# Kernel tuning notes

Hardware: AMD Instinct MI355X
Metric: run time of the kernel (lower is better)

The kernel has to match this reference:

```python
import jax, jax.numpy as jnp
import numpy as np

B, T, N, F = 4, 24, 1024, 96
H, HD = 3, 32      # spatial GATConv: 3 heads, head-dim 32 (averaged -> 32 per branch, 3 branches -> 96)
GH, GHD = 4, 24    # GroupedGAT: 4 heads concatenated -> 96
E = 8192           # edges per graph


def setup_inputs() -> dict:
    key = jax.random.key(0)
    ks = jax.random.split(key, 24)
    s_in = 1.0 / np.sqrt(F)
    def gat_params(k):
        k1, k2, k3, k4 = jax.random.split(k, 4)
        return (jax.random.normal(k1, (F, H * HD), jnp.float32) * s_in,
                jax.random.normal(k2, (H, HD), jnp.float32) * 0.1,
                jax.random.normal(k3, (H, HD), jnp.float32) * 0.1,
                jax.random.normal(k4, (H, HD), jnp.float32) * 0.02)
    W_d, al_d, ar_d, b_d = gat_params(ks[3])
    W_m, al_m, ar_m, b_m = gat_params(ks[4])
    W_s, al_s, ar_s, b_s = gat_params(ks[5])
    inp = {
        "input": jax.random.normal(ks[0], (B, T, N, F), jnp.float32),
        "spatial_embedding": jax.random.normal(ks[1], (B, T, N, F), jnp.float32),
        "temporal_embedding": jax.random.normal(ks[2], (B, T, N, F), jnp.float32),
        "src_d": jax.random.randint(ks[6], (E,), 0, N, jnp.int32),
        "dst_d": (jnp.arange(E) % N).astype(jnp.int32),
        "src_m": jax.random.randint(ks[7], (E,), 0, N, jnp.int32),
        "dst_m": (jnp.arange(E) % N).astype(jnp.int32),
        "src_s": jax.random.randint(ks[8], (E,), 0, N, jnp.int32),
        "dst_s": (jnp.arange(E) % N).astype(jnp.int32),
        "W_d": W_d, "al_d": al_d, "ar_d": ar_d, "b_d": b_d,
        "W_m": W_m, "al_m": al_m, "ar_m": ar_m, "b_m": b_m,
        "W_s": W_s, "al_s": al_s, "ar_s": ar_s, "b_s": b_s,
        "Wg": jax.random.normal(ks[9], (F, GH * GHD), jnp.float32) * s_in,
        "agl": jax.random.normal(ks[10], (GH, GHD), jnp.float32) * 0.1,
        "agr": jax.random.normal(ks[11], (GH, GHD), jnp.float32) * 0.1,
        "Wf": jax.random.normal(ks[12], (2 * F, F), jnp.float32) * (1.0 / np.sqrt(2 * F)),
        "bf": jnp.zeros((F,), jnp.float32),
    }
    return inp


def _gat(x, src, dst, W, al, ar, b):
    # x: (N, K, F) node features with K = T*B batched feature slots
    K = x.shape[1]
    h = (x @ W).reshape(N, K, H, HD)                       # (N,K,H,HD)
    el = (h * al).sum(-1)                                  # (N,K,H)
    er = (h * ar).sum(-1)
    e = jax.nn.leaky_relu(el[src] + er[dst], 0.2)          # (E,K,H)
    emax = jax.ops.segment_max(e, dst, num_segments=N)
    emax = jnp.where(jnp.isfinite(emax), emax, 0.0)
    ex = jnp.exp(e - emax[dst])
    denom = jax.ops.segment_sum(ex, dst, num_segments=N)
    alpha = ex / (denom[dst] + 1e-9)                       # edge softmax over incoming edges
    out = jax.ops.segment_sum(h[src] * alpha[..., None], dst, num_segments=N)
    return (out + b).mean(2)                               # average heads -> (N,K,HD)


def reference(input, spatial_embedding, temporal_embedding,
              src_d, dst_d, src_m, dst_m, src_s, dst_s,
              W_d, al_d, ar_d, b_d, W_m, al_m, ar_m, b_m, W_s, al_s, ar_s, b_s,
              Wg, agl, agr, Wf, bf):
    # ---------------- SpatialBlock ----------------
    residual_s = input                                     # input_dim == output_dim
    x_in = input + spatial_embedding
    # torch: input.transpose(0,2).reshape(N,-1,F) -> slot order is (t,b)
    x = jnp.transpose(x_in, (2, 1, 0, 3)).reshape(N, T * B, F)
    xd = _gat(x, src_d, dst_d, W_d, al_d, ar_d, b_d)
    xm = _gat(x, src_m, dst_m, W_m, al_m, ar_m, b_m)
    xs = _gat(x, src_s, dst_s, W_s, al_s, ar_s, b_s)
    x_attn = jnp.concatenate([xd, xm, xs], axis=-1)        # (N, T*B, 3*HD=F)
    # torch: transpose(0,1).reshape(batch,T,N,-1)  (keeps original (t,b) slot order quirk)
    x_attn = jnp.transpose(x_attn, (1, 0, 2)).reshape(B, T, N, F)
    cov0 = spatial_embedding[:, 0]                         # (B,N,F)
    attn_S = jax.nn.softmax(cov0 @ jnp.swapaxes(cov0, 1, 2), axis=2)  # (B,N,N)
    # NOTE: embedding_x branch in SpatialBlock is dead code (out is overwritten); skipped.
    spatial = residual_s + x_attn

    # ---------------- TemporalBlock ----------------
    residual_t = input
    xt = jnp.swapaxes(input, 1, 2).reshape(B * N, T, F)    # (B*N, T, F), index k=b*N+n
    # GroupedGAT: dense multi-head GAT over the T=period_num time steps
    hg = (xt @ Wg).reshape(B * N, T, GH, GHD)
    elg = (hg * agl).sum(-1)                               # (BN,T,GH)
    erg = (hg * agr).sum(-1)
    eg = jax.nn.leaky_relu(elg[:, :, None, :] + erg[:, None, :, :], 0.2)  # (BN,Ti,Tj,GH)
    alphag = jax.nn.softmax(eg, axis=2)
    xg = jnp.einsum('kijh,kjhd->kihd', alphag, hg).reshape(B * N, T, GH * GHD)
    covT = temporal_embedding[:, :, 0]                     # (B,T,F)
    attn_T = jax.nn.softmax(covT @ jnp.swapaxes(covT, 1, 2), axis=1)      # softmax over dim=1 as in torch
    # torch: attn.repeat(N,1,1) paired with x of batch index b*N+n -> uses attn[(b*N+n) % B]
    idx = (jnp.arange(B * N) % B)
    emb = jnp.einsum('kij,kjf->kif', attn_T[idx], xt)      # (BN,T,F)
    xg = xg * jax.nn.sigmoid(emb)
    xg = jnp.swapaxes(xg.reshape(B, N, T, F), 1, 2)        # (B,T,N,F)
    temporal = residual_t + xg

    # ---------------- Fusion ----------------
    z = jax.nn.sigmoid(jnp.concatenate([spatial, temporal], axis=-1) @ Wf + bf)
    out = z * spatial + (1.0 - z) * temporal + input
    return out, attn_S
```

## Files before the change

kernel.cpp:

```cpp
#include <hip/hip_runtime.h>
#include <hip/hip_bf16.h>

typedef long long i64;
typedef __attribute__((ext_vector_type(8))) short short8b;
typedef __attribute__((ext_vector_type(4))) short short4b;
typedef __attribute__((ext_vector_type(4))) float f32x4;

union U8 { short8b v; ushort s[8]; };
union U4 { short4b v; ushort s[4]; };

static __device__ __forceinline__ float bs2f(ushort u) {
    union { unsigned int i; float f; } x; x.i = ((unsigned int)u) << 16; return x.f;
}
static __device__ __forceinline__ ushort f2bs(float f) {
    __hip_bfloat16 h = __float2bfloat16(f);
    return *reinterpret_cast<ushort*>(&h);
}
static __device__ __forceinline__ void mfma_bf16(f32x4& acc, short8b a, short8b b) {
    asm volatile("v_mfma_f32_16x16x32_bf16 %0, %1, %2, %0" : "+v"(acc) : "v"(a), "v"(b));
}
static __device__ __forceinline__ void mfma_fence() {
    asm volatile("s_nop 7\n\ts_nop 7\n\ts_nop 7");
}


__global__ __launch_bounds__(256) void prep_weights_kernel(
        const float* __restrict__ Wd, const float* __restrict__ Wm,
        const float* __restrict__ Ws, const float* __restrict__ Wg,
        const float* __restrict__ Wf,
        const float* __restrict__ ald, const float* __restrict__ ard,
        const float* __restrict__ alm, const float* __restrict__ arm,
        const float* __restrict__ als, const float* __restrict__ ars,
        const float* __restrict__ agl, const float* __restrict__ agr,
        ushort* __restrict__ wtab) {
    int idx = blockIdx.x * 256 + threadIdx.x;
    if (idx >= 61440) return;
    if (idx < 43008) {
        int w = idx / 10752, rem = idx - w * 10752;
        int c = rem / 96, k = rem - c * 96;
        float v;
        if (w < 3) {
            const float* W = (w == 0) ? Wd : (w == 1) ? Wm : Ws;
            if (c < 96) {
                v = W[k * 96 + c];
            } else {
                int j = c - 96, h = j >> 1;
                const float* a = (j & 1) ? ((w == 0) ? ard : (w == 1) ? arm : ars)
                                         : ((w == 0) ? ald : (w == 1) ? alm : als);
                v = 0.f;
                for (int d = 0; d < 32; ++d) v += W[k * 96 + h * 32 + d] * a[h * 32 + d];
            }
        } else {
            if (c < 96) {
                v = Wg[k * 96 + c];
            } else {
                int j = c - 96, g = j & 3;
                const float* a = (j >> 2) ? agr : agl;
                v = 0.f;
                for (int d = 0; d < 24; ++d) v += Wg[k * 96 + g * 24 + d] * a[g * 24 + d];
            }
        }
        wtab[w * 10752 + c * 96 + k] = f2bs(v);
    } else {
        int rem = idx - 43008;
        int c = rem / 192, k = rem - c * 192;
        wtab[43008 + c * 192 + k] = f2bs(Wf[k * 96 + c]);
    }
}

__global__ __launch_bounds__(256) void build_x_kernel(const float* __restrict__ inp,
                                                      const float* __restrict__ spat,
                                                      ushort* __restrict__ x) {
    int i4 = blockIdx.x * 256 + threadIdx.x;
    int q = i4 % 24;
    int r = i4 / 24;
    int n = r & 1023, bt = r >> 10;
    int t = bt % 24, b = bt / 24;
    int k = t * 4 + b;
    float4 a = ((const float4*)inp)[i4];
    float4 s = ((const float4*)spat)[i4];
    U4 u;
    u.s[0] = f2bs(a.x + s.x); u.s[1] = f2bs(a.y + s.y);
    u.s[2] = f2bs(a.z + s.z); u.s[3] = f2bs(a.w + s.w);
    *(short4b*)&x[((i64)((k << 10) | n)) * 96 + q * 4] = u.v;
}

__global__ __launch_bounds__(256) void gemm96_mfma_kernel(const ushort* __restrict__ X,
                                                          const ushort* __restrict__ wt,
                                                          ushort* __restrict__ Ho,
                                                          float* __restrict__ el,
                                                          float* __restrict__ er) {
    __shared__ ushort Xs[128 * 104];
    __shared__ ushort Wt[112 * 104];
    int tid = threadIdx.x;
    i64 row0 = (i64)blockIdx.x * 128;
    for (int i = tid; i < 1344; i += 256) {
        int c = i / 12, kg = i - c * 12;
        *(short8b*)&Wt[c * 104 + kg * 8] = *(const short8b*)&wt[c * 96 + kg * 8];
    }
    for (int i = tid; i < 1536; i += 256) {
        int r = i / 12, q = i - r * 12;
        *(short8b*)&Xs[r * 104 + q * 8] = *(const short8b*)&X[(row0 + r) * 96 + q * 8];
    }
    __syncthreads();
    int wid = tid >> 6, lane = tid & 63;
    int lr = lane & 15, lk = lane >> 4;
    f32x4 acc[2][7];
#pragma unroll
    for (int m = 0; m < 2; ++m)
#pragma unroll
        for (int c = 0; c < 7; ++c) acc[m][c] = (f32x4){0.f, 0.f, 0.f, 0.f};
    const ushort* xa = &Xs[(wid * 32 + lr) * 104 + lk * 8];
    const ushort* wb = &Wt[lr * 104 + lk * 8];
#pragma unroll
    for (int ks = 0; ks < 3; ++ks) {
        short8b a0 = *(const short8b*)(xa + ks * 32);
        short8b a1 = *(const short8b*)(xa + 16 * 104 + ks * 32);
#pragma unroll
        for (int c = 0; c < 7; ++c) {
            short8b b = *(const short8b*)(wb + c * 16 * 104 + ks * 32);
            mfma_bf16(acc[0][c], a0, b);
            mfma_bf16(acc[1][c], a1, b);
        }
    }
    mfma_fence();
#pragma unroll
    for (int m = 0; m < 2; ++m) {
#pragma unroll
        for (int c = 0; c < 6; ++c)
#pragma unroll
            for (int r = 0; r < 4; ++r) {
                i64 row = row0 + wid * 32 + m * 16 + lk * 4 + r;
                Ho[row * 96 + c * 16 + lr] = f2bs(acc[m][c][r]);
            }
        if (lr < 6) {
            float* dst = (lr & 1) ? er : el;
            int h = lr >> 1;
#pragma unroll
            for (int r = 0; r < 4; ++r) {
                i64 row = row0 + wid * 32 + m * 16 + lk * 4 + r;
                dst[row * 3 + h] = acc[m][6][r];
            }
        }
    }
}

__global__ __launch_bounds__(256) void gemm96_hg_mfma_kernel(const float* __restrict__ inp,
                                                             const ushort* __restrict__ wt,
                                                             ushort* __restrict__ Ho,
                                                             float* __restrict__ elg,
                                                             float* __restrict__ erg) {
    __shared__ ushort Xs[128 * 104];
    __shared__ ushort Wt[112 * 104];
    int tid = threadIdx.x;
    i64 row0 = (i64)blockIdx.x * 128;
    for (int i = tid; i < 1344; i += 256) {
        int c = i / 12, kg = i - c * 12;
        *(short8b*)&Wt[c * 104 + kg * 8] = *(const short8b*)&wt[c * 96 + kg * 8];
    }
    for (int i = tid; i < 3072; i += 256) {
        int r = i / 24, q = i - r * 24;
        int row = (int)row0 + r;
        int kk = row / 24, t = row - kk * 24;
        int b = kk >> 10, n = kk & 1023;
        float4 v = ((const float4*)inp)[((i64)(((b * 24 + t) << 10) | n)) * 24 + q];
        U4 u;
        u.s[0] = f2bs(v.x); u.s[1] = f2bs(v.y); u.s[2] = f2bs(v.z); u.s[3] = f2bs(v.w);
        *(short4b*)&Xs[r * 104 + q * 4] = u.v;
    }
    __syncthreads();
    int wid = tid >> 6, lane = tid & 63;
    int lr = lane & 15, lk = lane >> 4;
    f32x4 acc[2][7];
#pragma unroll
    for (int m = 0; m < 2; ++m)
#pragma unroll
        for (int c = 0; c < 7; ++c) acc[m][c] = (f32x4){0.f, 0.f, 0.f, 0.f};
    const ushort* xa = &Xs[(wid * 32 + lr) * 104 + lk * 8];
    const ushort* wb = &Wt[lr * 104 + lk * 8];
#pragma unroll
    for (int ks = 0; ks < 3; ++ks) {
        short8b a0 = *(const short8b*)(xa + ks * 32);
        short8b a1 = *(const short8b*)(xa + 16 * 104 + ks * 32);
#pragma unroll
        for (int c = 0; c < 7; ++c) {
            short8b b = *(const short8b*)(wb + c * 16 * 104 + ks * 32);
            mfma_bf16(acc[0][c], a0, b);
            mfma_bf16(acc[1][c], a1, b);
        }
    }
    mfma_fence();
#pragma unroll
    for (int m = 0; m < 2; ++m) {
#pragma unroll
        for (int c = 0; c < 6; ++c)
#pragma unroll
            for (int r = 0; r < 4; ++r) {
                i64 row = row0 + wid * 32 + m * 16 + lk * 4 + r;
                Ho[row * 96 + c * 16 + lr] = f2bs(acc[m][c][r]);
            }
        if (lr < 8) {
            float* dst = (lr >> 2) ? erg : elg;
            int g = lr & 3;
#pragma unroll
            for (int r = 0; r < 4; ++r) {
                i64 row = row0 + wid * 32 + m * 16 + lk * 4 + r;
                dst[row * 4 + g] = acc[m][6][r];
            }
        }
    }
}

__global__ __launch_bounds__(256) void gat_agg_kernel(const ushort* __restrict__ H2,
                                                      const float* __restrict__ el,
                                                      const float* __restrict__ er,
                                                      const int* __restrict__ src,
                                                      const float* __restrict__ bv,
                                                      ushort* __restrict__ xattn,
                                                      int g) {
    int tid = threadIdx.x;
    int pp = tid >> 3, l8 = tid & 7;
    int p = blockIdx.x * 32 + pp;
    int k = p >> 10, n = p & 1023;
    int d0 = l8 * 4;
    i64 kb = (i64)(k << 10);
    int s_own = src[n + l8 * 1024];
    const float* elp = &el[(kb | s_own) * 3];
    const float* erp = &er[(kb | n) * 3];
    float e[3], m[3];
#pragma unroll
    for (int h = 0; h < 3; ++h) {
        float ev = elp[h] + erp[h];
        e[h] = ev >= 0.f ? ev : 0.2f * ev;
        m[h] = e[h];
    }
#pragma unroll
    for (int mask = 1; mask < 8; mask <<= 1) {
#pragma unroll
        for (int h = 0; h < 3; ++h) m[h] = fmaxf(m[h], __shfl_xor(m[h], mask, 8));
    }
    float pex[3], S[3];
#pragma unroll
    for (int h = 0; h < 3; ++h) { pex[h] = expf(e[h] - m[h]); S[h] = pex[h]; }
#pragma unroll
    for (int mask = 1; mask < 8; mask <<= 1) {
#pragma unroll
        for (int h = 0; h < 3; ++h) S[h] += __shfl_xor(S[h], mask, 8);
    }
    float w[3];
#pragma unroll
    for (int h = 0; h < 3; ++h) w[h] = pex[h] / (S[h] + 1e-9f);
    float acc[4] = {0.f, 0.f, 0.f, 0.f};
#pragma unroll
    for (int j = 0; j < 8; ++j) {
        int sj = __shfl(s_own, j, 8);
        float a0 = __shfl(w[0], j, 8);
        float a1 = __shfl(w[1], j, 8);
        float a2 = __shfl(w[2], j, 8);
        const ushort* hp = &H2[(kb | sj) * 96 + d0];
        U4 h0, h1, h2;
        h0.v = *(const short4b*)&hp[0];
        h1.v = *(const short4b*)&hp[32];
        h2.v = *(const short4b*)&hp[64];
#pragma unroll
        for (int c = 0; c < 4; ++c)
            acc[c] += a0 * bs2f(h0.s[c]) + a1 * bs2f(h1.s[c]) + a2 * bs2f(h2.s[c]);
    }
    float4 b0 = *(const float4*)&bv[d0];
    float4 b1 = *(const float4*)&bv[32 + d0];
    float4 b2 = *(const float4*)&bv[64 + d0];
    float bsum[4] = {b0.x + b1.x + b2.x, b0.y + b1.y + b2.y,
                     b0.z + b1.z + b2.z, b0.w + b1.w + b2.w};
    U4 u;
#pragma unroll
    for (int c = 0; c < 4; ++c) u.s[c] = f2bs((acc[c] + bsum[c]) * (1.f / 3.f));
    *(short4b*)&xattn[(kb | n) * 96 + g * 32 + d0] = u.v;
}

__global__ __launch_bounds__(256) void attn_scores_kernel(const float* __restrict__ spat,
                                                          float* __restrict__ attnS) {
    int bid = blockIdx.x;
    int b = bid >> 8;
    int i0 = ((bid >> 4) & 15) * 64;
    int j0 = (bid & 15) * 64;
    const float* C = spat + (i64)b * 24 * 1024 * 96;
    __shared__ __align__(16) float As[64 * 100];
    __shared__ __align__(16) float Bs[64 * 100];
    int tid = threadIdx.x;
    float4* As4 = (float4*)As;
    float4* Bs4 = (float4*)Bs;
    const float4* Ai = (const float4*)(C + (i64)i0 * 96);
    const float4* Bj = (const float4*)(C + (i64)j0 * 96);
    for (int i = tid; i < 1536; i += 256) {
        int row = i / 24, q = i - row * 24;
        As4[row * 25 + q] = Ai[i];
        Bs4[row * 25 + q] = Bj[i];
    }
    __syncthreads();
    int tj = tid & 15, ti = tid >> 4;
    float acc[4][4];
#pragma unroll
    for (int r = 0; r < 4; ++r)
#pragma unroll
        for (int s = 0; s < 4; ++s) acc[r][s] = 0.f;
    for (int k4 = 0; k4 < 24; ++k4) {
        float4 a[4], bv[4];
#pragma unroll
        for (int r = 0; r < 4; ++r) a[r] = As4[(ti * 4 + r) * 25 + k4];
#pragma unroll
        for (int s = 0; s < 4; ++s) bv[s] = Bs4[(s * 16 + tj) * 25 + k4];
#pragma unroll
        for (int r = 0; r < 4; ++r)
#pragma unroll
            for (int s = 0; s < 4; ++s)
                acc[r][s] += a[r].x * bv[s].x + a[r].y * bv[s].y + a[r].z * bv[s].z + a[r].w * bv[s].w;
    }
#pragma unroll
    for (int r = 0; r < 4; ++r) {
        i64 orow = ((i64)(b << 10) + i0 + ti * 4 + r) * 1024 + j0;
#pragma unroll
        for (int s = 0; s < 4; ++s) attnS[orow + s * 16 + tj] = acc[r][s];
    }
}

__global__ __launch_bounds__(256) void attn_softmax_kernel(float* __restrict__ attnS) {
    i64 base = (i64)blockIdx.x * 1024;
    float4* row4 = (float4*)(attnS + base);
    int tid = threadIdx.x;
    float4 v = row4[tid];
    __shared__ float red[256];
    float m = fmaxf(fmaxf(v.x, v.y), fmaxf(v.z, v.w));
    red[tid] = m;
    __syncthreads();
    for (int st = 128; st > 0; st >>= 1) {
        if (tid < st) red[tid] = fmaxf(red[tid], red[tid + st]);
        __syncthreads();
    }
    m = red[0];
    __syncthreads();
    v.x = expf(v.x - m); v.y = expf(v.y - m); v.z = expf(v.z - m); v.w = expf(v.w - m);
    red[tid] = v.x + v.y + v.z + v.w;
    __syncthreads();
    for (int st = 128; st > 0; st >>= 1) {
        if (tid < st) red[tid] += red[tid + st];
        __syncthreads();
    }
    float inv = 1.f / red[0];
    v.x *= inv; v.y *= inv; v.z *= inv; v.w *= inv;
    row4[tid] = v;
}

__global__ __launch_bounds__(576) void attn_t_kernel(const float* __restrict__ temp,
                                                     float* __restrict__ attnT) {
    int b = blockIdx.x;
    int tid = threadIdx.x;
    __shared__ float cs[24][96];
    __shared__ float M[24][24];
    for (int i = tid; i < 2304; i += 576) {
        int r = i / 96, f = i - r * 96;
        cs[r][f] = temp[((i64)(b * 24 + r)) * 1024 * 96 + f];
    }
    __syncthreads();
    int i = tid / 24, j = tid - i * 24;
    float s = 0.f;
#pragma unroll
    for (int f = 0; f < 96; ++f) s += cs[i][f] * cs[j][f];
    M[i][j] = s;
    __syncthreads();
    float m = -1e30f;
#pragma unroll
    for (int i2 = 0; i2 < 24; ++i2) m = fmaxf(m, M[i2][j]);
    float sum = 0.f;
#pragma unroll
    for (int i2 = 0; i2 < 24; ++i2) sum += expf(M[i2][j] - m);
    attnT[((i64)b * 24 + i) * 24 + j] = expf(M[i][j] - m) / sum;
}

__global__ __launch_bounds__(576) void sig_kernel(const float* __restrict__ inp,
                                                  const float* __restrict__ attnT,
                                                  ushort* __restrict__ sig) {
    int kk = blockIdx.x;
    int b = kk >> 10, n = kk & 1023;
    __shared__ __align__(16) float xs[24 * 100];
    __shared__ float ats[576];
    int tid = threadIdx.x;
    {
        int r = tid / 24, q = tid - (tid / 24) * 24;
        *(float4*)&xs[r * 100 + q * 4] =
            ((const float4*)inp)[(((i64)(b * 24 + r)) << 10 | n) * 24 + q];
        ats[tid] = attnT[(kk & 3) * 576 + tid];
    }
    __syncthreads();
    int i = tid / 24, f4 = tid - (tid / 24) * 24;
    const float* ap = &ats[i * 24];
    float4 acc = {0.f, 0.f, 0.f, 0.f};
#pragma unroll
    for (int j = 0; j < 24; ++j) {
        float a = ap[j];
        float4 v = *(const float4*)&xs[j * 100 + f4 * 4];
        acc.x += a * v.x; acc.y += a * v.y; acc.z += a * v.z; acc.w += a * v.w;
    }
    U4 o;
    o.s[0] = f2bs(1.f / (1.f + expf(-acc.x)));
    o.s[1] = f2bs(1.f / (1.f + expf(-acc.y)));
    o.s[2] = f2bs(1.f / (1.f + expf(-acc.z)));
    o.s[3] = f2bs(1.f / (1.f + expf(-acc.w)));
    *(short4b*)&sig[(i64)kk * 2304 + i * 96 + f4 * 4] = o.v;
}

__global__ __launch_bounds__(192) void xg_kernel(const ushort* __restrict__ hg,
                                                 const float* __restrict__ elgb,
                                                 const float* __restrict__ ergb,
                                                 const ushort* __restrict__ sig,
                                                 ushort* __restrict__ gated) {
    int kk = blockIdx.x;
    __shared__ __align__(16) ushort hgs[24 * 96];
    __shared__ __align__(16) float alphaT[4 * 24 * 32];
    __shared__ __align__(16) float elg[24][4], erg[24][4];
    int tid = threadIdx.x;
    for (int i = tid; i < 576; i += 192)
        *(short4b*)&hgs[i * 4] = *(const short4b*)&hg[(i64)kk * 2304 + i * 4];
    for (int i = tid; i < 48; i += 192) {
        int r = i >> 1;
        if (i & 1) *(float4*)&erg[r][0] = ((const float4*)ergb)[(i64)kk * 24 + r];
        else       *(float4*)&elg[r][0] = ((const float4*)elgb)[(i64)kk * 24 + r];
    }
    __syncthreads();
    {
        int i = tid >> 3, g = (tid >> 1) & 3, half = tid & 1;
        int j0 = half * 12;
        float eli = elg[i][g];
        float ev[12];
        float m = -1e30f;
#pragma unroll
        for (int j = 0; j < 12; ++j) {
            float e = eli + erg[j0 + j][g];
            e = e >= 0.f ? e : 0.2f * e;
            ev[j] = e;
            m = fmaxf(m, e);
        }
        m = fmaxf(m, __shfl_xor(m, 1));
        float sum = 0.f;
#pragma unroll
        for (int j = 0; j < 12; ++j) { ev[j] = expf(ev[j] - m); sum += ev[j]; }
        sum += __shfl_xor(sum, 1);
        float inv = 1.f / sum;
        int slot = ((i / 3) * 4 + (i - (i / 3) * 3)) ^ (g << 3);
#pragma unroll
        for (int j = 0; j < 12; ++j) alphaT[g * 768 + (j0 + j) * 32 + slot] = ev[j] * inv;
    }
    __syncthreads();
    int ig = tid / 24, f4 = tid - (tid / 24) * 24;
    int g = f4 / 6;
    float4 xg0 = {0,0,0,0}, xg1 = {0,0,0,0}, xg2 = {0,0,0,0};
    const float* aT = &alphaT[g * 768 + ((ig * 4) ^ (g << 3))];
#pragma unroll
    for (int j = 0; j < 24; ++j) {
        U4 uh; uh.v = *(const short4b*)&hgs[j * 96 + f4 * 4];
        float4 a4 = *(const float4*)&aT[j * 32];
        float h0 = bs2f(uh.s[0]), h1 = bs2f(uh.s[1]), h2 = bs2f(uh.s[2]), h3 = bs2f(uh.s[3]);
        xg0.x += a4.x * h0; xg0.y += a4.x * h1; xg0.z += a4.x * h2; xg0.w += a4.x * h3;
        xg1.x += a4.y * h0; xg1.y += a4.y * h1; xg1.z += a4.y * h2; xg1.w += a4.y * h3;
        xg2.x += a4.z * h0; xg2.y += a4.z * h1; xg2.z += a4.z * h2; xg2.w += a4.z * h3;
    }
    i64 obase = (i64)kk * 2304 + f4 * 4;
#pragma unroll
    for (int r = 0; r < 3; ++r) {
        float4 xg = (r == 0) ? xg0 : (r == 1) ? xg1 : xg2;
        i64 off = obase + (i64)(ig * 3 + r) * 96;
        U4 us; us.v = *(const short4b*)&sig[off];
        U4 o;
        o.s[0] = f2bs(xg.x * bs2f(us.s[0]));
        o.s[1] = f2bs(xg.y * bs2f(us.s[1]));
        o.s[2] = f2bs(xg.z * bs2f(us.s[2]));
        o.s[3] = f2bs(xg.w * bs2f(us.s[3]));
        *(short4b*)&gated[off] = o.v;
    }
}

__global__ __launch_bounds__(384) void fusion_mfma_kernel(const float* __restrict__ inp,
                                                          const ushort* __restrict__ xattn,
                                                          const ushort* __restrict__ gated,
                                                          const ushort* __restrict__ wtf,
                                                          const float* __restrict__ bfv,
                                                          float* __restrict__ outb) {
    extern __shared__ __align__(16) ushort dynlds[];
    ushort* Xs = dynlds;
    ushort* Wt = dynlds + 96 * 200;
    float* zbuf = (float*)Wt;
    int tid = threadIdx.x;
    i64 row0 = (i64)blockIdx.x * 96;
    for (int i = tid; i < 2304; i += 384) {
        int c = i / 24, kg = i - c * 24;
        *(short8b*)&Wt[c * 200 + kg * 8] = *(const short8b*)&wtf[c * 192 + kg * 8];
    }
    for (int i = tid; i < 1152; i += 384) {
        int r = i / 12, q = i - r * 12;
        i64 grow = row0 + r;
        int n = (int)(grow & 1023);
        int bt = (int)(grow >> 10);
        int t = bt % 24, b = bt / 24;
        float4 iv0 = ((const float4*)inp)[grow * 24 + q * 2];
        float4 iv1 = ((const float4*)inp)[grow * 24 + q * 2 + 1];
        U8 xa; xa.v = *(const short8b*)&xattn[grow * 96 + q * 8];
        U8 gd; gd.v = *(const short8b*)&gated[(((i64)((b << 10) | n)) * 24 + t) * 96 + q * 8];
        float ivf[8] = {iv0.x, iv0.y, iv0.z, iv0.w, iv1.x, iv1.y, iv1.z, iv1.w};
        U8 sp, tm;
#pragma unroll
        for (int j = 0; j < 8; ++j) {
            sp.s[j] = f2bs(ivf[j] + bs2f(xa.s[j]));
            tm.s[j] = f2bs(ivf[j] + bs2f(gd.s[j]));
        }
        *(short8b*)&Xs[r * 200 + q * 8] = sp.v;
        *(short8b*)&Xs[r * 200 + 96 + q * 8] = tm.v;
    }
    __syncthreads();
    int wid = tid >> 6, lane = tid & 63;
    int lr = lane & 15, lk = lane >> 4;
    f32x4 acc[6];
#pragma unroll
    for (int c = 0; c < 6; ++c) acc[c] = (f32x4){0.f, 0.f, 0.f, 0.f};
    const ushort* xa = &Xs[(wid * 16 + lr) * 200 + lk * 8];
    const ushort* wb = &Wt[lr * 200 + lk * 8];
#pragma unroll
    for (int ks = 0; ks < 6; ++ks) {
        short8b a = *(const short8b*)(xa + ks * 32);
#pragma unroll
        for (int c = 0; c < 6; ++c) {
            short8b b = *(const short8b*)(wb + c * 16 * 200 + ks * 32);
            mfma_bf16(acc[c], a, b);
        }
    }
    mfma_fence();
    __syncthreads();
#pragma unroll
    for (int c = 0; c < 6; ++c) {
        int col = c * 16 + lr;
        float bfc = bfv[col];
#pragma unroll
        for (int r = 0; r < 4; ++r) {
            int lrow = wid * 16 + lk * 4 + r;
            zbuf[lrow * 100 + col] = 1.f / (1.f + expf(-(acc[c][r] + bfc)));
        }
    }
    __syncthreads();
    for (int i = tid; i < 2304; i += 384) {
        int r2 = i / 24, q = i - r2 * 24;
        i64 grow = row0 + r2;
        float4 iv = ((const float4*)inp)[grow * 24 + q];
        float4 zv = *(const float4*)&zbuf[r2 * 100 + q * 4];
        U4 spv; spv.v = *(const short4b*)&Xs[r2 * 200 + q * 4];
        U4 tmv; tmv.v = *(const short4b*)&Xs[r2 * 200 + 96 + q * 4];
        float4 o;
        o.x = zv.x * bs2f(spv.s[0]) + (1.f - zv.x) * bs2f(tmv.s[0]) + iv.x;
        o.y = zv.y * bs2f(spv.s[1]) + (1.f - zv.y) * bs2f(tmv.s[1]) + iv.y;
        o.z = zv.z * bs2f(spv.s[2]) + (1.f - zv.z) * bs2f(tmv.s[2]) + iv.z;
        o.w = zv.w * bs2f(spv.s[3]) + (1.f - zv.w) * bs2f(tmv.s[3]) + iv.w;
        ((float4*)outb)[grow * 24 + q] = o;
    }
}

extern "C" void kernel_launch(void* const* d_in, const int* in_sizes, int n_in,
                              void* d_out, int out_size, void* d_ws, size_t ws_size,
                              hipStream_t stream) {
    const float* input = (const float*)d_in[0];
    const float* spat  = (const float*)d_in[1];
    const float* temp  = (const float*)d_in[2];
    const int* src_d = (const int*)d_in[3];
    const int* src_m = (const int*)d_in[5];
    const int* src_s = (const int*)d_in[7];
    const float* W_d  = (const float*)d_in[9];
    const float* al_d = (const float*)d_in[10];
    const float* ar_d = (const float*)d_in[11];
    const float* b_d  = (const float*)d_in[12];
    const float* W_m  = (const float*)d_in[13];
    const float* al_m = (const float*)d_in[14];
    const float* ar_m = (const float*)d_in[15];
    const float* b_m  = (const float*)d_in[16];
    const float* W_s  = (const float*)d_in[17];
    const float* al_s = (const float*)d_in[18];
    const float* ar_s = (const float*)d_in[19];
    const float* b_s  = (const float*)d_in[20];
    const float* Wg   = (const float*)d_in[21];
    const float* agl  = (const float*)d_in[22];
    const float* agr  = (const float*)d_in[23];
    const float* Wf   = (const float*)d_in[24];
    const float* bf_  = (const float*)d_in[25];

    float* outb  = (float*)d_out;
    float* attnS = outb + 9437184;

    float* wsf = (float*)d_ws;
    ushort* xbf      = (ushort*)wsf;
    ushort* hgbf     = xbf;
    ushort* H2bf     = (ushort*)(wsf + 4718592);
    ushort* gatedbf  = H2bf;
    ushort* xattnbf  = (ushort*)(wsf + 9437184);
    float* el    = wsf + 14155776;
    float* er    = el + 294912;
    float* elgb  = wsf + 14155776;
    float* attnT = wsf + 14745600;
    float* ergb  = wsf + 14747904;
    ushort* wtab = (ushort*)(wsf + 15141120);
    ushort* wt_d = wtab;
    ushort* wt_m = wtab + 10752;
    ushort* wt_s = wtab + 21504;
    ushort* wtg  = wtab + 32256;
    ushort* wtf  = wtab + 43008;
    ushort* sigbf = (ushort*)outb;

    static int attr_set = 0;
    if (!attr_set) {
        hipFuncSetAttribute((const void*)fusion_mfma_kernel,
                            hipFuncAttributeMaxDynamicSharedMemorySize, 76800);
        attr_set = 1;
    }

    prep_weights_kernel<<<240, 256, 0, stream>>>(W_d, W_m, W_s, Wg, Wf,
                                                 al_d, ar_d, al_m, ar_m, al_s, ar_s,
                                                 agl, agr, wtab);
    build_x_kernel<<<9216, 256, 0, stream>>>(input, spat, xbf);

    const ushort* Wgat[3] = {wt_d, wt_m, wt_s};
    const float* bgat[3] = {b_d, b_m, b_s};
    const int* srcs[3] = {src_d, src_m, src_s};
    for (int g = 0; g < 3; ++g) {
        gemm96_mfma_kernel<<<768, 256, 0, stream>>>(xbf, Wgat[g], H2bf, el, er);
        gat_agg_kernel<<<3072, 256, 0, stream>>>(H2bf, el, er, srcs[g], bgat[g],
                                                 xattnbf, g);
    }

    attn_scores_kernel<<<1024, 256, 0, stream>>>(spat, attnS);
    attn_softmax_kernel<<<4096, 256, 0, stream>>>(attnS);

    attn_t_kernel<<<4, 576, 0, stream>>>(temp, attnT);
    sig_kernel<<<4096, 576, 0, stream>>>(input, attnT, sigbf);
    gemm96_hg_mfma_kernel<<<768, 256, 0, stream>>>(input, wtg, hgbf, elgb, ergb);
    xg_kernel<<<4096, 192, 0, stream>>>(hgbf, elgb, ergb, sigbf, gatedbf);
    fusion_mfma_kernel<<<1024, 384, 76800, stream>>>(input, xattnbf, gatedbf, wtf,
                                                     bf_, outb);
}
```

Measured before the change: 245.6 us.

## Fuse temporal attention into sig kernel, widen score tiles, vectorize el/er loads

Pads the GAT el/er arrays to stride 4 so the aggregation kernel reads them with single float4 loads. Enlarges the attention-score tile to 128x64 rows per block using dynamic shared memory, halving the grid. Removes the separate temporal-attention kernel by recomputing the 24x24 softmax inside each sig_kernel block. Prefetches input rows in the fusion epilogue before the barrier. This saves launches and memory traffic, but adds redundant per-block compute and register pressure.

```diff
diff --git a/kernel.cpp b/kernel.cpp
--- a/kernel.cpp
+++ b/kernel.cpp
@@ -139,7 +139,7 @@
 #pragma unroll
             for (int r = 0; r < 4; ++r) {
                 i64 row = row0 + wid * 32 + m * 16 + lk * 4 + r;
-                dst[row * 3 + h] = acc[m][6][r];
+                dst[row * 4 + h] = acc[m][6][r];
             }
         }
     }
@@ -225,14 +225,15 @@
     int d0 = l8 * 4;
     i64 kb = (i64)(k << 10);
     int s_own = src[n + l8 * 1024];
-    const float* elp = &el[(kb | s_own) * 3];
-    const float* erp = &er[(kb | n) * 3];
+    float4 elv = *(const float4*)&el[(kb | s_own) * 4];
+    float4 erv = *(const float4*)&er[(kb | n) * 4];
     float e[3], m[3];
-#pragma unroll
-    for (int h = 0; h < 3; ++h) {
-        float ev = elp[h] + erp[h];
-        e[h] = ev >= 0.f ? ev : 0.2f * ev;
-        m[h] = e[h];
+    {
+        float ev0 = elv.x + erv.x, ev1 = elv.y + erv.y, ev2 = elv.z + erv.z;
+        e[0] = ev0 >= 0.f ? ev0 : 0.2f * ev0;
+        e[1] = ev1 >= 0.f ? ev1 : 0.2f * ev1;
+        e[2] = ev2 >= 0.f ? ev2 : 0.2f * ev2;
+        m[0] = e[0]; m[1] = e[1]; m[2] = e[2];
     }
 #pragma unroll
     for (int mask = 1; mask < 8; mask <<= 1) {
@@ -279,45 +280,50 @@
 
 __global__ __launch_bounds__(256) void attn_scores_kernel(const float* __restrict__ spat,
                                                           float* __restrict__ attnS) {
+    extern __shared__ __align__(16) float dynf[];
+    float* As = dynf;
+    float* Bs = dynf + 12800;
     int bid = blockIdx.x;
-    int b = bid >> 8;
-    int i0 = ((bid >> 4) & 15) * 64;
-    int j0 = (bid & 15) * 64;
+    int b = bid >> 7;
+    int it = (bid >> 4) & 7;
+    int jt = bid & 15;
+    int i0 = it * 128, j0 = jt * 64;
     const float* C = spat + (i64)b * 24 * 1024 * 96;
-    __shared__ __align__(16) float As[64 * 100];
-    __shared__ __align__(16) float Bs[64 * 100];
     int tid = threadIdx.x;
     float4* As4 = (float4*)As;
     float4* Bs4 = (float4*)Bs;
     const float4* Ai = (const float4*)(C + (i64)i0 * 96);
     const float4* Bj = (const float4*)(C + (i64)j0 * 96);
+    for (int i = tid; i < 3072; i += 256) {
+        int row = i / 24, q = i - row * 24;
+        As4[row * 25 + q] = Ai[i];
+    }
     for (int i = tid; i < 1536; i += 256) {
         int row = i / 24, q = i - row * 24;
-        As4[row * 25 + q] = Ai[i];
         Bs4[row * 25 + q] = Bj[i];
     }
     __syncthreads();
     int tj = tid & 15, ti = tid >> 4;
-    float acc[4][4];
-#pragma unroll
-    for (int r = 0; r < 4; ++r)
+    float acc[8][4];
+#pragma unroll
+    for (int r = 0; r < 8; ++r)
 #pragma unroll
         for (int s = 0; s < 4; ++s) acc[r][s] = 0.f;
     for (int k4 = 0; k4 < 24; ++k4) {
-        float4 a[4], bv[4];
-#pragma unroll
-        for (int r = 0; r < 4; ++r) a[r] = As4[(ti * 4 + r) * 25 + k4];
+        float4 a[8], bv[4];
+#pragma unroll
+        for (int r = 0; r < 8; ++r) a[r] = As4[(ti * 8 + r) * 25 + k4];
 #pragma unroll
         for (int s = 0; s < 4; ++s) bv[s] = Bs4[(s * 16 + tj) * 25 + k4];
 #pragma unroll
-        for (int r = 0; r < 4; ++r)
+        for (int r = 0; r < 8; ++r)
 #pragma unroll
             for (int s = 0; s < 4; ++s)
                 acc[r][s] += a[r].x * bv[s].x + a[r].y * bv[s].y + a[r].z * bv[s].z + a[r].w * bv[s].w;
     }
 #pragma unroll
-    for (int r = 0; r < 4; ++r) {
-        i64 orow = ((i64)(b << 10) + i0 + ti * 4 + r) * 1024 + j0;
+    for (int r = 0; r < 8; ++r) {
+        i64 orow = ((i64)(b << 10) + i0 + ti * 8 + r) * 1024 + j0;
 #pragma unroll
         for (int s = 0; s < 4; ++s) attnS[orow + s * 16 + tj] = acc[r][s];
     }
@@ -350,54 +356,50 @@
     row4[tid] = v;
 }
 
-__global__ __launch_bounds__(576) void attn_t_kernel(const float* __restrict__ temp,
-                                                     float* __restrict__ attnT) {
-    int b = blockIdx.x;
-    int tid = threadIdx.x;
-    __shared__ float cs[24][96];
-    __shared__ float M[24][24];
-    for (int i = tid; i < 2304; i += 576) {
-        int r = i / 96, f = i - r * 96;
-        cs[r][f] = temp[((i64)(b * 24 + r)) * 1024 * 96 + f];
-    }
-    __syncthreads();
-    int i = tid / 24, j = tid - i * 24;
-    float s = 0.f;
-#pragma unroll
-    for (int f = 0; f < 96; ++f) s += cs[i][f] * cs[j][f];
-    M[i][j] = s;
-    __syncthreads();
-    float m = -1e30f;
-#pragma unroll
-    for (int i2 = 0; i2 < 24; ++i2) m = fmaxf(m, M[i2][j]);
-    float sum = 0.f;
-#pragma unroll
-    for (int i2 = 0; i2 < 24; ++i2) sum += expf(M[i2][j] - m);
-    attnT[((i64)b * 24 + i) * 24 + j] = expf(M[i][j] - m) / sum;
-}
-
 __global__ __launch_bounds__(576) void sig_kernel(const float* __restrict__ inp,
-                                                  const float* __restrict__ attnT,
+                                                  const float* __restrict__ temp,
                                                   ushort* __restrict__ sig) {
     int kk = blockIdx.x;
-    int b = kk >> 10, n = kk & 1023;
+    int b = kk >> 10, n = kk & 1023, ib = kk & 3;
     __shared__ __align__(16) float xs[24 * 100];
+    __shared__ __align__(16) float cs[24 * 100];
+    __shared__ float M[576];
     __shared__ float ats[576];
     int tid = threadIdx.x;
+    int r = tid / 24, q = tid - r * 24;
+    ((float4*)xs)[r * 25 + q] =
+        ((const float4*)inp)[(((i64)(b * 24 + r)) << 10 | n) * 24 + q];
+    ((float4*)cs)[r * 25 + q] =
+        ((const float4*)temp)[(i64)(ib * 24 + r) * 24576 + q];
+    __syncthreads();
     {
-        int r = tid / 24, q = tid - (tid / 24) * 24;
-        *(float4*)&xs[r * 100 + q * 4] =
-            ((const float4*)inp)[(((i64)(b * 24 + r)) << 10 | n) * 24 + q];
-        ats[tid] = attnT[(kk & 3) * 576 + tid];
-    }
-    __syncthreads();
-    int i = tid / 24, f4 = tid - (tid / 24) * 24;
-    const float* ap = &ats[i * 24];
+        const float4* ci = (const float4*)cs + r * 25;
+        const float4* cj = (const float4*)cs + q * 25;
+        float s = 0.f;
+#pragma unroll
+        for (int kq = 0; kq < 24; ++kq) {
+            float4 a = ci[kq], c = cj[kq];
+            s += a.x * c.x + a.y * c.y + a.z * c.z + a.w * c.w;
+        }
+        M[r * 24 + q] = s;
+    }
+    __syncthreads();
+    {
+        float m = -1e30f;
+#pragma unroll
+        for (int i2 = 0; i2 < 24; ++i2) m = fmaxf(m, M[i2 * 24 + q]);
+        float sum = 0.f;
+#pragma unroll
+        for (int i2 = 0; i2 < 24; ++i2) sum += expf(M[i2 * 24 + q] - m);
+        ats[r * 24 + q] = expf(M[r * 24 + q] - m) / sum;
+    }
+    __syncthreads();
+    const float* ap = &ats[r * 24];
     float4 acc = {0.f, 0.f, 0.f, 0.f};
 #pragma unroll
     for (int j = 0; j < 24; ++j) {
         float a = ap[j];
-        float4 v = *(const float4*)&xs[j * 100 + f4 * 4];
+        float4 v = *(const float4*)&xs[j * 100 + q * 4];
         acc.x += a * v.x; acc.y += a * v.y; acc.z += a * v.z; acc.w += a * v.w;
     }
     U4 o;
@@ -405,7 +407,7 @@
     o.s[1] = f2bs(1.f / (1.f + expf(-acc.y)));
     o.s[2] = f2bs(1.f / (1.f + expf(-acc.z)));
     o.s[3] = f2bs(1.f / (1.f + expf(-acc.w)));
-    *(short4b*)&sig[(i64)kk * 2304 + i * 96 + f4 * 4] = o.v;
+    *(short4b*)&sig[(i64)kk * 2304 + r * 96 + q * 4] = o.v;
 }
 
 __global__ __launch_bounds__(192) void xg_kernel(const ushort* __restrict__ hg,
@@ -532,6 +534,13 @@
         }
     }
     mfma_fence();
+    float4 ivp[6];
+#pragma unroll
+    for (int ii = 0; ii < 6; ++ii) {
+        int i = tid + ii * 384;
+        int r2 = i / 24, q = i - r2 * 24;
+        ivp[ii] = ((const float4*)inp)[(row0 + r2) * 24 + q];
+    }
     __syncthreads();
 #pragma unroll
     for (int c = 0; c < 6; ++c) {
@@ -544,10 +553,12 @@
         }
     }
     __syncthreads();
-    for (int i = tid; i < 2304; i += 384) {
+#pragma unroll
+    for (int ii = 0; ii < 6; ++ii) {
+        int i = tid + ii * 384;
         int r2 = i / 24, q = i - r2 * 24;
         i64 grow = row0 + r2;
-        float4 iv = ((const float4*)inp)[grow * 24 + q];
+        float4 iv = ivp[ii];
         float4 zv = *(const float4*)&zbuf[r2 * 100 + q * 4];
         U4 spv; spv.v = *(const short4b*)&Xs[r2 * 200 + q * 4];
         U4 tmv; tmv.v = *(const short4b*)&Xs[r2 * 200 + 96 + q * 4];
@@ -597,11 +608,10 @@
     ushort* gatedbf  = H2bf;
     ushort* xattnbf  = (ushort*)(wsf + 9437184);
     float* el    = wsf + 14155776;
-    float* er    = el + 294912;
-    float* elgb  = wsf + 14155776;
-    float* attnT = wsf + 14745600;
-    float* ergb  = wsf + 14747904;
-    ushort* wtab = (ushort*)(wsf + 15141120);
+    float* er    = wsf + 14548992;
+    float* elgb  = el;
+    float* ergb  = er;
+    ushort* wtab = (ushort*)(wsf + 14942208);
     ushort* wt_d = wtab;
     ushort* wt_m = wtab + 10752;
     ushort* wt_s = wtab + 21504;
@@ -612,6 +622,8 @@
     static int attr_set = 0;
     if (!attr_set) {
         hipFuncSetAttribute((const void*)fusion_mfma_kernel,
+                            hipFuncAttributeMaxDynamicSharedMemorySize, 76800);
+        hipFuncSetAttribute((const void*)attn_scores_kernel,
                             hipFuncAttributeMaxDynamicSharedMemorySize, 76800);
         attr_set = 1;
     }
@@ -630,11 +642,10 @@
                                                  xattnbf, g);
     }
 
-    attn_scores_kernel<<<1024, 256, 0, stream>>>(spat, attnS);
+    attn_scores_kernel<<<512, 256, 76800, stream>>>(spat, attnS);
     attn_softmax_kernel<<<4096, 256, 0, stream>>>(attnS);
 
-    attn_t_kernel<<<4, 576, 0, stream>>>(temp, attnT);
-    sig_kernel<<<4096, 576, 0, stream>>>(input, attnT, sigbf);
+    sig_kernel<<<4096, 576, 0, stream>>>(input, temp, sigbf);
     gemm96_hg_mfma_kernel<<<768, 256, 0, stream>>>(input, wtg, hgbf, elgb, ergb);
     xg_kernel<<<4096, 192, 0, stream>>>(hgbf, elgb, ergb, sigbf, gatedbf);
     fusion_mfma_kernel<<<1024, 384, 76800, stream>>>(input, xattnbf, gatedbf, wtf,
```

New measurement: 287.4 us. 1.17x slower.
